# Optimization experiments

Hardware: AMD Instinct MI355X
Metric: run time of the kernel (lower is better)

Reference implementation:

```python
import jax, jax.numpy as jnp
import numpy as np

D = 128           # embed_dim
NUM_LAYERS = 2
N_CLASSES = 4
OUT_CELL = 64
SPEAKERS = 2
INPUT_DIMS = [768, 74, 35]
B, T = 32, 60


def setup_inputs() -> dict:
    key = jax.random.key(0)
    ks = jax.random.split(key, 24)
    inp = {}
    inp['x0'] = jax.random.normal(ks[0], (B, T, INPUT_DIMS[0]), jnp.float32)
    inp['x1'] = jax.random.normal(ks[1], (B, T, INPUT_DIMS[1]), jnp.float32)
    inp['x2'] = jax.random.normal(ks[2], (B, T, INPUT_DIMS[2]), jnp.float32)
    inp['smask'] = jax.random.normal(ks[3], (B, T, SPEAKERS), jnp.float32)  # argmax -> speaker ids
    # modality projections
    for i, d in enumerate(INPUT_DIMS):
        inp[f'Wp{i}'] = jax.random.normal(ks[4 + i], (d, D), jnp.float32) / np.float32(np.sqrt(d))
        inp[f'bp{i}'] = jnp.zeros((D,), jnp.float32)
    # shared PositionEmbedding (ModuleList([m]*3) shares params)
    inp['freq_emb'] = jax.random.normal(ks[7], (SPEAKERS, D), jnp.float32) * 0.1
    inp['phase_emb'] = jax.random.normal(ks[8], (SPEAKERS, D), jnp.float32)
    # shared QRNNCell (ModuleList([cell]*num_layers) shares params)
    inp['U_x'] = jnp.linalg.qr(jax.random.normal(ks[9], (D, D), jnp.float32))[0]
    inp['U_h'] = jnp.linalg.qr(jax.random.normal(ks[10], (D, D), jnp.float32))[0]
    inp['Lambda'] = jnp.float32(0.5)
    # QMeasurement kernel (real/imag parts of D measurement vectors)
    inp['kernel_r'] = jnp.eye(D, dtype=jnp.float32) + 0.05 * jax.random.normal(ks[11], (D, D), jnp.float32)
    inp['kernel_i'] = 0.05 * jax.random.normal(ks[12], (D, D), jnp.float32)
    # SimpleNet fc_out
    inp['W1'] = jax.random.normal(ks[13], (D, OUT_CELL), jnp.float32) / np.float32(np.sqrt(D))
    inp['b1'] = jnp.zeros((OUT_CELL,), jnp.float32)
    inp['W2'] = jax.random.normal(ks[14], (OUT_CELL, N_CLASSES), jnp.float32) / np.float32(np.sqrt(OUT_CELL))
    inp['b2'] = jnp.zeros((N_CLASSES,), jnp.float32)
    return inp


def _qmn_forward(x0, x1, x2, smask, Wp0, bp0, Wp1, bp1, Wp2, bp2,
                 freq_emb, phase_emb, U_x, U_h, Lambda,
                 kernel_r, kernel_i, W1, b1, W2, b2):
    xs = [x0, x1, x2]
    Ws = [(Wp0, bp0), (Wp1, bp1), (Wp2, bp2)]
    reps = [jax.nn.relu(x @ W + b) for x, (W, b) in zip(xs, Ws)]           # [B,T,D] each
    # mixture weights: softmax over per-modality L2 norms
    norms = jnp.concatenate([jnp.linalg.norm(r, axis=-1, keepdims=True) for r in reps], axis=-1)
    weights = jax.nn.softmax(norms, axis=-1)                               # [B,T,M]
    # shared phase embedding: phase = t * freq[speaker] + phase[speaker]
    ids = jnp.argmax(smask, axis=-1)                                       # [B,T] int
    pos = jnp.arange(T, dtype=jnp.float32)[None, :, None]                  # [1,T,1]
    phase = pos * freq_emb[ids] + phase_emb[ids]                           # [B,T,D]
    cosp, sinp = jnp.cos(phase), jnp.sin(phase)
    # mixed density matrices rho = sum_m w_m |v_m><v_m|
    rho_r = jnp.zeros((B, T, D, D), jnp.float32)
    rho_i = jnp.zeros((B, T, D, D), jnp.float32)
    for m, r in enumerate(reps):
        a = r / jnp.maximum(jnp.linalg.norm(r, axis=-1, keepdims=True), 1e-12)
        pr = a * cosp                                                       # real amplitude
        pi = a * sinp                                                       # imag amplitude
        w = weights[..., m][..., None, None]
        rho_r = rho_r + w * (jnp.einsum('btm,btn->btmn', pr, pr) + jnp.einsum('btm,btn->btmn', pi, pi))
        rho_i = rho_i + w * (jnp.einsum('btm,btn->btmn', pi, pr) - jnp.einsum('btm,btn->btmn', pr, pi))
    # time-major for scan
    sr = jnp.transpose(rho_r, (1, 0, 2, 3))                                # [T,B,D,D]
    si = jnp.transpose(rho_i, (1, 0, 2, 3))

    def cell(h, x):
        hr, hi = h
        xr, xi = x
        Xr = jnp.einsum('mp,bpq,nq->bmn', U_x, xr, U_x)
        Xi = jnp.einsum('mp,bpq,nq->bmn', U_x, xi, U_x)
        Hr = jnp.einsum('mp,bpq,nq->bmn', U_h, hr, U_h)
        Hi = jnp.einsum('mp,bpq,nq->bmn', U_h, hi, U_h)
        nr = Lambda * Hr + (1.0 - Lambda) * Xr
        ni = Lambda * Hi + (1.0 - Lambda) * Xi
        return (nr, ni), (nr, ni)

    h0 = (jnp.broadcast_to(jnp.eye(D, dtype=jnp.float32) / D, (B, D, D)),
          jnp.zeros((B, D, D), jnp.float32))
    for _ in range(NUM_LAYERS):  # same shared cell params each layer
        _, (sr, si) = jax.lax.scan(cell, h0, (sr, si))
    # QMeasurement: p_k = Re(v_k^dag rho v_k), unit-norm complex measurement vectors
    nrm = jnp.sqrt(jnp.sum(kernel_r**2 + kernel_i**2, axis=1, keepdims=True))
    vr = kernel_r / jnp.maximum(nrm, 1e-12)                                # [K,D], K=D
    vi = kernel_i / jnp.maximum(nrm, 1e-12)
    probs = (jnp.einsum('tbmn,km,kn->tbk', sr, vr, vr)
             + jnp.einsum('tbmn,km,kn->tbk', sr, vi, vi)
             - jnp.einsum('tbmn,km,kn->tbk', si, vr, vi)
             + jnp.einsum('tbmn,km,kn->tbk', si, vi, vr))                  # [T,B,D]
    # SimpleNet (dropout = identity at inference)
    hid = jax.nn.relu(probs @ W1 + b1)
    out = jnp.tanh(hid @ W2 + b2)                                          # [T,B,C]
    out = jnp.transpose(out, (1, 0, 2))                                    # [B,T,C]
    return jax.nn.log_softmax(out, axis=2)


def reference(x0, x1, x2, smask, Wp0, bp0, Wp1, bp1, Wp2, bp2,
              freq_emb, phase_emb, U_x, U_h, Lambda,
              kernel_r, kernel_i, W1, b1, W2, b2):
    return _qmn_forward(x0, x1, x2, smask, Wp0, bp0, Wp1, bp1, Wp2, bp2,
                        freq_emb, phase_emb, U_x, U_h, Lambda,
                        kernel_r, kernel_i, W1, b1, W2, b2)
```

## Files before the change

kernel.cpp:

```cpp
#include <hip/hip_runtime.h>


#define DB 32
#define DT 60
#define DD 128
#define BT (DB*DT)
#define SP 136

typedef unsigned short ushort_t;
typedef __attribute__((ext_vector_type(8))) __bf16 bf16x8;
typedef __attribute__((ext_vector_type(8))) unsigned short ushort8_t;
typedef __attribute__((ext_vector_type(4))) float  float4v;

__device__ __forceinline__ float bf2f(ushort_t u){
  union { unsigned int i; float f; } x; x.i = ((unsigned int)u) << 16; return x.f;
}
__device__ __forceinline__ ushort_t f2bf(float f){
  union { float f; unsigned int i; } x; x.f = f;
  unsigned int lsb = (x.i >> 16) & 1u;
  return (ushort_t)((x.i + 0x7FFFu + lsb) >> 16);
}
__device__ __forceinline__ unsigned int f2bfpk(float a, float b){
#if defined(__gfx950__) && __has_builtin(__builtin_amdgcn_cvt_pk_bf16_f32)
  auto v = __builtin_amdgcn_cvt_pk_bf16_f32(a, b);
  unsigned int r; __builtin_memcpy(&r, &v, 4); return r;
#else
  return (unsigned int)f2bf(a) | ((unsigned int)f2bf(b) << 16);
#endif
}
__device__ __forceinline__ void split2(float v, ushort_t& h, ushort_t& l){
  h = f2bf(v); l = f2bf(v - bf2f(h));
}

template<int RT, int CT, bool ALO, bool BLO>
__device__ __forceinline__ void gemm_t(const ushort_t* Ah, const ushort_t* Al,
                                       const ushort_t* Bh, const ushort_t* Bl,
                                       float4v* acc, int row0, int col0, int gma, int q)
{
  for (int ks = 0; ks < 4; ks++){
    int ko = ks*32 + q*8;
    bf16x8 aF[RT], aL[RT], bF[CT], bL[CT];
    #pragma unroll
    for (int R = 0; R < RT; R++){
      int row = row0 + 16*R + gma;
      aF[R] = *(const bf16x8*)&Ah[row*SP + ko];
      if (ALO) aL[R] = *(const bf16x8*)&Al[row*SP + ko];
    }
    #pragma unroll
    for (int C = 0; C < CT; C++){
      int row = col0 + 16*C + gma;
      bF[C] = *(const bf16x8*)&Bh[row*SP + ko];
      if (BLO) bL[C] = *(const bf16x8*)&Bl[row*SP + ko];
    }
    #pragma unroll
    for (int R = 0; R < RT; R++)
      #pragma unroll
      for (int C = 0; C < CT; C++){
        float4v c = acc[R*CT+C];
        c = __builtin_amdgcn_mfma_f32_16x16x32_bf16(aF[R], bF[C], c, 0, 0, 0);
        if (BLO) c = __builtin_amdgcn_mfma_f32_16x16x32_bf16(aF[R], bL[C], c, 0, 0, 0);
        if (ALO) c = __builtin_amdgcn_mfma_f32_16x16x32_bf16(aL[R], bF[C], c, 0, 0, 0);
        acc[R*CT+C] = c;
      }
  }
}

template<int RT, int CT>
__device__ __forceinline__ void emit_t(const float4v* acc, ushort_t* dst, int stride,
                                       int row0, int col0, int gma, int q){
  #pragma unroll
  for (int R = 0; R < RT; R++)
    #pragma unroll
    for (int C = 0; C < CT; C++){
      int c = col0 + 16*C + gma, r0 = row0 + 16*R + 4*q;
      uint2 o;
      o.x = f2bfpk(acc[R*CT+C][0], acc[R*CT+C][1]);
      o.y = f2bfpk(acc[R*CT+C][2], acc[R*CT+C][3]);
      *(uint2*)&dst[(size_t)c*stride + r0] = o;
    }
}
template<int RT, int CT>
__device__ __forceinline__ void emit_split_t(const float4v* acc, ushort_t* dh, ushort_t* dl, int stride,
                                             int row0, int col0, int gma, int q){
  #pragma unroll
  for (int R = 0; R < RT; R++)
    #pragma unroll
    for (int C = 0; C < CT; C++){
      int c = col0 + 16*C + gma, r0 = row0 + 16*R + 4*q;
      ushort4 hh, ll;
      split2(acc[R*CT+C][0], hh.x, ll.x); split2(acc[R*CT+C][1], hh.y, ll.y);
      split2(acc[R*CT+C][2], hh.z, ll.z); split2(acc[R*CT+C][3], hh.w, ll.w);
      *(ushort4*)&dh[(size_t)c*stride + r0] = hh;
      *(ushort4*)&dl[(size_t)c*stride + r0] = ll;
    }
}
template<int NT>
__device__ __forceinline__ void lds_load_mat(ushort_t* dst, const ushort_t* src, int tid){
  for (int i = tid*8; i < 16384; i += NT*8){
    int r = i >> 7, k = i & 127;
    *(ushort8_t*)&dst[r*SP + k] = *(const ushort8_t*)&src[i];
  }
}
template<int NT>
__device__ __forceinline__ void lds_load_rows16(ushort_t* dst, const ushort_t* src, int tid){
  for (int i = tid*8; i < 2048; i += NT*8){
    int r = i >> 7, k = i & 127;
    *(ushort8_t*)&dst[r*SP + k] = *(const ushort8_t*)&src[i];
  }
}
template<int NT>
__device__ __forceinline__ void lds_load_mat2(ushort_t* d0, const ushort_t* s0,
                                              ushort_t* d1, const ushort_t* s1, int tid){
  constexpr int CH = 16384/(NT*8);
  ushort8_t r0[CH], r1[CH];
  #pragma unroll
  for (int c = 0; c < CH; c++) r0[c] = *(const ushort8_t*)&s0[tid*8 + c*NT*8];
  #pragma unroll
  for (int c = 0; c < CH; c++) r1[c] = *(const ushort8_t*)&s1[tid*8 + c*NT*8];
  #pragma unroll
  for (int c = 0; c < CH; c++){
    int i = tid*8 + c*NT*8; int r = i >> 7, k = i & 127;
    *(ushort8_t*)&d0[r*SP + k] = r0[c];
  }
  #pragma unroll
  for (int c = 0; c < CH; c++){
    int i = tid*8 + c*NT*8; int r = i >> 7, k = i & 127;
    *(ushort8_t*)&d1[r*SP + k] = r1[c];
  }
}
template<int NT>
__device__ __forceinline__ void lds_store_mat(ushort_t* dst, const ushort_t* src, int tid){
  for (int i = tid*8; i < 16384; i += NT*8){
    int r = i >> 7, k = i & 127;
    *(ushort8_t*)&dst[i] = *(const ushort8_t*)&src[r*SP + k];
  }
}

__global__ void k_small(const float* Ux, const float* Uh, const float* kr, const float* ki,
                        const float* Wp0, const float* Wp1, const float* Wp2,
                        const float* x0, const float* x1, const float* x2,
                        ushort_t* UxTh, ushort_t* UxTl, ushort_t* UxH, ushort_t* UxL,
                        float* Vr, float* Vi,
                        ushort_t* PpH, ushort_t* PpL, ushort_t* PTh, ushort_t* PTl,
                        ushort_t* WT0h, ushort_t* WT0l, ushort_t* WT1h, ushort_t* WT1l,
                        ushort_t* WT2h, ushort_t* WT2l,
                        ushort_t* X0h, ushort_t* X0l, ushort_t* X1h, ushort_t* X1l,
                        ushort_t* X2h, ushort_t* X2l){
  int blk = blockIdx.x, d = threadIdx.x;
  if (blk < 128){
    int i = blk;
    float v = Ux[i*DD + d];
    ushort_t h, l; split2(v, h, l);
    UxTh[d*DD + i] = h; UxTl[d*DD + i] = l;
  } else if (blk < 256){
    __shared__ float red[DD];
    int k = blk - 128;
    float r = kr[k*DD+d], im = ki[k*DD+d];
    red[d] = r*r + im*im;
    __syncthreads();
    for (int s = 64; s > 0; s >>= 1){ if (d < s) red[d] += red[d+s]; __syncthreads(); }
    float nrm = fmaxf(sqrtf(red[0]), 1e-12f);
    Vr[k*DD+d] = r/nrm; Vi[k*DD+d] = im/nrm;
  } else if (blk < 384){
    int i = blk - 256;
    float v = Uh[i*DD + d];
    ushort_t h, l; split2(v, h, l);
    PpH[i*DD + d] = h;  PpL[i*DD + d] = l;
    PTh[d*DD + i] = h;  PTl[d*DD + i] = l;
  } else if (blk < 512){
    int dd2 = blk - 384;
    ushort_t h, l;
    for (int k = d; k < 768; k += 128){
      split2(Wp0[(size_t)k*DD + dd2], h, l);
      WT0h[(size_t)dd2*768 + k] = h; WT0l[(size_t)dd2*768 + k] = l;
    }
    { float v = (d < 74) ? Wp1[(size_t)d*DD + dd2] : 0.f;
      split2(v, h, l); WT1h[dd2*128 + d] = h; WT1l[dd2*128 + d] = l; }
    { float v = (d < 35) ? Wp2[(size_t)d*DD + dd2] : 0.f;
      split2(v, h, l); WT2h[dd2*128 + d] = h; WT2l[dd2*128 + d] = l; }
    { split2(Ux[(size_t)dd2*DD + d], h, l);
      UxH[dd2*DD + d] = h; UxL[dd2*DD + d] = l; }
  } else {
    int bt = blk - 512;
    ushort_t h, l;
    const float* r0 = x0 + (size_t)bt*768;
    #pragma unroll
    for (int j = 0; j < 6; j++){
      split2(r0[j*128 + d], h, l);
      X0h[(size_t)bt*768 + j*128 + d] = h;
      X0l[(size_t)bt*768 + j*128 + d] = l;
    }
    float v1 = (d < 74) ? x1[(size_t)bt*74 + d] : 0.f;
    split2(v1, h, l);
    X1h[(size_t)bt*128 + d] = h; X1l[(size_t)bt*128 + d] = l;
    float v2 = (d < 35) ? x2[(size_t)bt*35 + d] : 0.f;
    split2(v2, h, l);
    X2h[(size_t)bt*128 + d] = h; X2l[(size_t)bt*128 + d] = l;
  }
}

__global__ __launch_bounds__(512,1) void k_proj(
    const ushort_t* X0h, const ushort_t* X0l, const ushort_t* X1h, const ushort_t* X1l,
    const ushort_t* X2h, const ushort_t* X2l,
    const ushort_t* WT0h, const ushort_t* WT0l, const ushort_t* WT1h, const ushort_t* WT1l,
    const ushort_t* WT2h, const ushort_t* WT2l,
    const float* bp1, const float* bp2,
    float* Rpart, float* Reps)
{
  __shared__ ushort_t Ah[128*SP], Al[128*SP], Bh[128*SP], Bl[128*SP];
  int blk = blockIdx.x;
  int m, tile, ch;
  if (blk < 90){ m = 0; tile = blk/6; ch = blk%6; }
  else if (blk < 105){ m = 1; tile = blk-90; ch = 0; }
  else { m = 2; tile = blk-105; ch = 0; }
  int bt0 = tile*128;
  int tid = threadIdx.x;
  int w = tid >> 6, lane = tid & 63, gma = lane & 15, q = lane >> 4;
  int row0 = 32*(w >> 1), col0 = 64*(w & 1);
  const ushort_t* Wh_ = (m==0)? WT0h : (m==1)? WT1h : WT2h;
  const ushort_t* Wl_ = (m==0)? WT0l : (m==1)? WT1l : WT2l;
  const ushort_t* Xh_ = (m==0)? X0h : (m==1)? X1h : X2h;
  const ushort_t* Xl_ = (m==0)? X0l : (m==1)? X1l : X2l;
  int KX = (m==0)? 768 : 128;
  for (int i = tid*8; i < 16384; i += 4096){
    int r = i >> 7, k = i & 127;
    *(ushort8_t*)&Ah[r*SP + k] = *(const ushort8_t*)&Wh_[(size_t)r*KX + ch*128 + k];
    *(ushort8_t*)&Al[r*SP + k] = *(const ushort8_t*)&Wl_[(size_t)r*KX + ch*128 + k];
    *(ushort8_t*)&Bh[r*SP + k] = *(const ushort8_t*)&Xh_[(size_t)(bt0+r)*KX + ch*128 + k];
    *(ushort8_t*)&Bl[r*SP + k] = *(const ushort8_t*)&Xl_[(size_t)(bt0+r)*KX + ch*128 + k];
  }
  __syncthreads();
  float4v acc[8];
  #pragma unroll
  for (int i = 0; i < 8; i++) acc[i] = (float4v){0.f,0.f,0.f,0.f};
  gemm_t<2,4,true,true>(Ah, Al, Bh, Bl, acc, row0, col0, gma, q);
  if (m == 0){
    #pragma unroll
    for (int R = 0; R < 2; R++)
      #pragma unroll
      for (int C = 0; C < 4; C++){
        int c = col0 + 16*C + gma, r0 = row0 + 16*R + 4*q;
        float4 o;
        o.x = acc[R*4+C][0]; o.y = acc[R*4+C][1];
        o.z = acc[R*4+C][2]; o.w = acc[R*4+C][3];
        *(float4*)&Rpart[((size_t)ch*BT + bt0 + c)*128 + r0] = o;
      }
  } else {
    const float* bp = (m==1)? bp1 : bp2;
    #pragma unroll
    for (int R = 0; R < 2; R++){
      int r0 = row0 + 16*R + 4*q;
      float4 bv = *(const float4*)&bp[r0];
      #pragma unroll
      for (int C = 0; C < 4; C++){
        int c = col0 + 16*C + gma;
        float4v a = acc[R*4+C];
        float4 o;
        o.x = fmaxf(a[0]+bv.x, 0.f); o.y = fmaxf(a[1]+bv.y, 0.f);
        o.z = fmaxf(a[2]+bv.z, 0.f); o.w = fmaxf(a[3]+bv.w, 0.f);
        *(float4*)&Reps[(size_t)(bt0 + c)*384 + m*128 + r0] = o;
      }
    }
  }
}

__global__ __launch_bounds__(128) void k_mix(const float* Rpart, const float* Reps,
    const float* bp0, const float* smask,
    const float* freq, const float* phem, ushort_t* PsH, ushort_t* PsL, float* Wgt)
{
  __shared__ float part[2][3];
  int bt = blockIdx.x; int t = bt % DT;
  int d = threadIdx.x;
  float r0v = bp0[d];
  #pragma unroll
  for (int ch = 0; ch < 6; ch++)
    r0v += Rpart[((size_t)ch*BT + bt)*128 + d];
  r0v = fmaxf(r0v, 0.f);
  float r1v = Reps[(size_t)bt*384 + 128 + d];
  float r2v = Reps[(size_t)bt*384 + 256 + d];
  float s0 = r0v*r0v, s1 = r1v*r1v, s2 = r2v*r2v;
  #pragma unroll
  for (int off = 1; off < 64; off <<= 1){
    s0 += __shfl_xor(s0, off, 64);
    s1 += __shfl_xor(s1, off, 64);
    s2 += __shfl_xor(s2, off, 64);
  }
  int wv = d >> 6;
  if ((d & 63) == 0){ part[wv][0] = s0; part[wv][1] = s1; part[wv][2] = s2; }
  __syncthreads();
  float n0 = sqrtf(part[0][0] + part[1][0]);
  float n1 = sqrtf(part[0][1] + part[1][1]);
  float n2 = sqrtf(part[0][2] + part[1][2]);
  float mx = fmaxf(n0, fmaxf(n1, n2));
  float e0 = expf(n0-mx), e1 = expf(n1-mx), e2 = expf(n2-mx);
  float einv = 1.f/(e0+e1+e2);
  if (d < 3) Wgt[bt*3+d] = (d==0?e0:(d==1?e1:e2))*einv;
  float sm0 = smask[bt*2], sm1 = smask[bt*2+1];
  int id = (sm1 > sm0) ? 1 : 0;
  float ph = (float)t * freq[id*DD+d] + phem[id*DD+d];
  float cp = cosf(ph), sp = sinf(ph);
  float a0 = r0v / fmaxf(n0, 1e-12f);
  float a1 = r1v / fmaxf(n1, 1e-12f);
  float a2 = r2v / fmaxf(n2, 1e-12f);
  ushort_t h, l;
  split2(a0*cp, h, l); PsH[((size_t)0*BT + bt)*DD + d] = h; PsL[((size_t)0*BT + bt)*DD + d] = l;
  split2(a1*cp, h, l); PsH[((size_t)1*BT + bt)*DD + d] = h; PsL[((size_t)1*BT + bt)*DD + d] = l;
  split2(a2*cp, h, l); PsH[((size_t)2*BT + bt)*DD + d] = h; PsL[((size_t)2*BT + bt)*DD + d] = l;
  split2(a0*sp, h, l); PsH[((size_t)3*BT + bt)*DD + d] = h; PsL[((size_t)3*BT + bt)*DD + d] = l;
  split2(a1*sp, h, l); PsH[((size_t)4*BT + bt)*DD + d] = h; PsL[((size_t)4*BT + bt)*DD + d] = l;
  split2(a2*sp, h, l); PsH[((size_t)5*BT + bt)*DD + d] = h; PsL[((size_t)5*BT + bt)*DD + d] = l;
}

__global__ __launch_bounds__(512,1) void k_qtrans(const ushort_t* UxH, const ushort_t* UxL,
                                                  const ushort_t* PsH, const ushort_t* PsL,
                                                  ushort_t* Qb){
  __shared__ ushort_t Ah[128*SP], Al[128*SP], Bh[128*SP], Bl[128*SP];
  int blk = blockIdx.x;
  int tid = threadIdx.x;
  int w = tid >> 6, lane = tid & 63, gma = lane & 15, q = lane >> 4;
  int row0 = 32*(w >> 1), col0 = 64*(w & 1);
  size_t rbase = (size_t)blk*128*128;
  lds_load_mat<512>(Ah, UxH, tid);
  lds_load_mat<512>(Al, UxL, tid);
  lds_load_mat<512>(Bh, PsH + rbase, tid);
  lds_load_mat<512>(Bl, PsL + rbase, tid);
  __syncthreads();
  float4v acc[8];
  #pragma unroll
  for (int i = 0; i < 8; i++) acc[i] = (float4v){0.f,0.f,0.f,0.f};
  gemm_t<2,4,true,true>(Ah, Al, Bh, Bl, acc, row0, col0, gma, q);
  emit_t<2,4>(acc, Qb + rbase, 128, row0, col0, gma, q);
}

__global__ __launch_bounds__(256,2) void k_pow2v2(ushort_t* PpH, ushort_t* PpL,
                                                  ushort_t* PTh, ushort_t* PTl, int s){
  __shared__ ushort_t Ah[128*SP], Al[128*SP], Bh[16*SP], Bl[16*SP];
  int blk = blockIdx.x;
  int which = blk >> 3, sl = blk & 7;
  size_t src = (size_t)(s-1)*16384, dst = (size_t)s*16384;
  int tid = threadIdx.x;
  int w = tid >> 6, lane = tid & 63, gma = lane & 15, q = lane >> 4;
  int row0 = 32*w;
  int gcol0 = sl*16;
  const ushort_t *A_h, *A_l, *B_h, *B_l; ushort_t *D_h, *D_l;
  if (which == 0){ A_h = PTh+src; A_l = PTl+src; B_h = PpH+src; B_l = PpL+src;
                   D_h = PpH+dst; D_l = PpL+dst; }
  else           { A_h = PpH+src; A_l = PpL+src; B_h = PTh+src; B_l = PTl+src;
                   D_h = PTh+dst; D_l = PTl+dst; }
  lds_load_mat<256>(Ah, A_h, tid);
  lds_load_mat<256>(Al, A_l, tid);
  lds_load_rows16<256>(Bh, B_h + (size_t)gcol0*128, tid);
  lds_load_rows16<256>(Bl, B_l + (size_t)gcol0*128, tid);
  __syncthreads();
  float4v acc[2];
  acc[0] = (float4v){0.f,0.f,0.f,0.f};
  acc[1] = (float4v){0.f,0.f,0.f,0.f};
  gemm_t<2,1,true,true>(Ah, Al, Bh, Bl, acc, row0, 0, gma, q);
  emit_split_t<2,1>(acc, D_h, D_l, 128, row0, gcol0, gma, q);
}

__global__ __launch_bounds__(512,1) void k_gchain(const ushort_t* PpH, const ushort_t* PpL,
                                                  const ushort_t* PTh, const ushort_t* PTl,
                                                  ushort_t* GTh, ushort_t* GTl){
  __shared__ ushort_t Ah[128*SP], Al[128*SP], Bh[128*SP], Bl[128*SP];
  int t = blockIdx.x;
  int tid = threadIdx.x;
  int w = tid >> 6, lane = tid & 63, gma = lane & 15, q = lane >> 4;
  int row0 = 32*(w >> 1), col0 = 64*(w & 1);
  size_t gslot = (size_t)t * 16384;
  if (t == 0){
    for (int i = tid*4; i < 16384; i += 2048){
      int r = i >> 7, k = i & 127;
      ushort4 zz; zz.x = zz.y = zz.z = zz.w = 0;
      *(ushort4*)&GTl[gslot + i] = zz;
      ushort4 oh;
      oh.x = (r == (k+0)) ? (ushort_t)0x3F80 : (ushort_t)0;
      oh.y = (r == (k+1)) ? (ushort_t)0x3F80 : (ushort_t)0;
      oh.z = (r == (k+2)) ? (ushort_t)0x3F80 : (ushort_t)0;
      oh.w = (r == (k+3)) ? (ushort_t)0x3F80 : (ushort_t)0;
      *(ushort4*)&GTh[gslot + i] = oh;
    }
    return;
  }
  int b0 = __ffs(t) - 1;
  int rem = t & ~(1 << b0);
  if (rem == 0){
    size_t ps = (size_t)b0 * 16384;
    for (int i = tid*4; i < 16384; i += 2048){
      *(ushort4*)&GTh[gslot + i] = *(const ushort4*)&PTh[ps + i];
      *(ushort4*)&GTl[gslot + i] = *(const ushort4*)&PTl[ps + i];
    }
    return;
  }
  lds_load_mat<512>(Ah, PpH + (size_t)b0*16384, tid);
  lds_load_mat<512>(Al, PpL + (size_t)b0*16384, tid);
  while (rem){
    int k = __ffs(rem) - 1;
    rem &= ~(1 << k);
    lds_load_mat<512>(Bh, PTh + (size_t)k*16384, tid);
    lds_load_mat<512>(Bl, PTl + (size_t)k*16384, tid);
    __syncthreads();
    float4v acc[8];
    #pragma unroll
    for (int i = 0; i < 8; i++) acc[i] = (float4v){0.f,0.f,0.f,0.f};
    if (rem){
      gemm_t<2,4,true,true>(Bh, Bl, Ah, Al, acc, row0, col0, gma, q);
      __syncthreads();
      emit_split_t<2,4>(acc, Ah, Al, SP, row0, col0, gma, q);
      __syncthreads();
    } else {
      gemm_t<2,4,true,true>(Ah, Al, Bh, Bl, acc, row0, col0, gma, q);
      emit_split_t<2,4>(acc, GTh + gslot, GTl + gslot, 128, row0, col0, gma, q);
    }
  }
}

__global__ __launch_bounds__(256,1) void k_precompMW(const ushort_t* GTh, const ushort_t* GTl,
                                                     const ushort_t* UxTh, const ushort_t* UxTl,
                                                     const float* Vr, const float* Vi,
                                                     ushort_t* Mh, ushort_t* Wh){
  __shared__ ushort_t Bh[128*SP], Bl[128*SP], Ah[128*SP], Al[128*SP];
  int blk = blockIdx.x;
  int tid = threadIdx.x;
  int w = tid >> 6, lane = tid & 63, gma = lane & 15, q = lane >> 4;
  int row0 = 64*(w >> 1), col0 = 64*(w & 1);
  if (blk < 60){
    int t = blk;
    lds_load_mat<256>(Bh, GTh + (size_t)t*16384, tid);
    lds_load_mat<256>(Bl, GTl + (size_t)t*16384, tid);
    lds_load_mat<256>(Ah, UxTh, tid);
    lds_load_mat<256>(Al, UxTl, tid);
    __syncthreads();
    float4v acc[16];
    #pragma unroll
    for (int i = 0; i < 16; i++) acc[i] = (float4v){0.f,0.f,0.f,0.f};
    gemm_t<4,4,true,true>(Ah, Al, Bh, Bl, acc, row0, col0, gma, q);
    __syncthreads();
    emit_split_t<4,4>(acc, Ah, Al, SP, row0, col0, gma, q);
    __syncthreads();
    #pragma unroll
    for (int i = 0; i < 16; i++) acc[i] = (float4v){0.f,0.f,0.f,0.f};
    gemm_t<4,4,true,true>(Bh, Bl, Ah, Al, acc, row0, col0, gma, q);
    #pragma unroll
    for (int R = 0; R < 4; R++)
      #pragma unroll
      for (int C = 0; C < 4; C++){
        int c = col0 + 16*C + gma, r0 = row0 + 16*R + 4*q;
        uint2 o;
        o.x = f2bfpk(acc[R*4+C][0], acc[R*4+C][1]);
        o.y = f2bfpk(acc[R*4+C][2], acc[R*4+C][3]);
        *(uint2*)&Mh[(size_t)t*16384 + c*128 + r0] = o;
      }
  } else {
    int bx = blk - 60;
    int t = bx >> 1, which = bx & 1;
    lds_load_mat<256>(Ah, GTh + (size_t)t*16384, tid);
    lds_load_mat<256>(Al, GTl + (size_t)t*16384, tid);
    const float* V = which ? Vi : Vr;
    for (int i = tid; i < 16384; i += 256){
      int r = i >> 7, k = i & 127;
      ushort_t h, l; split2(V[i], h, l);
      Bh[r*SP + k] = h; Bl[r*SP + k] = l;
    }
    __syncthreads();
    float4v acc[16];
    #pragma unroll
    for (int i = 0; i < 16; i++) acc[i] = (float4v){0.f,0.f,0.f,0.f};
    gemm_t<4,4,true,true>(Ah, Al, Bh, Bl, acc, row0, col0, gma, q);
    #pragma unroll
    for (int R = 0; R < 4; R++)
      #pragma unroll
      for (int C = 0; C < 4; C++){
        int c = col0 + 16*C + gma, r0 = row0 + 16*R + 4*q;
        uint2 o;
        o.x = f2bfpk(acc[R*4+C][0], acc[R*4+C][1]);
        o.y = f2bfpk(acc[R*4+C][2], acc[R*4+C][3]);
        *(uint2*)&Wh[(size_t)bx*16384 + c*128 + r0] = o;
      }
  }
}

__global__ __launch_bounds__(512,1) void k_vtrans(const ushort_t* GTh, const ushort_t* Qb, ushort_t* At){
  __shared__ ushort_t Ah[128*SP];
  __shared__ ushort_t Bs[192*SP];
  int t = blockIdx.x;
  int tid = threadIdx.x;
  int w = tid >> 6, lane = tid & 63, gma = lane & 15, q = lane >> 4;
  int row0 = (w & 3)*32, col0 = (w >> 2)*96;
  lds_load_mat<512>(Ah, GTh + (size_t)t*16384, tid);
  for (int i = tid*8; i < 192*128; i += 4096){
    int m = i >> 7, k = i & 127;
    int j = m >> 5, b = m & 31;
    *(ushort8_t*)&Bs[m*SP + k] =
      *(const ushort8_t*)&Qb[((size_t)(j*BT) + b*DT + t)*DD + k];
  }
  __syncthreads();
  float4v acc[12];
  #pragma unroll
  for (int i = 0; i < 12; i++) acc[i] = (float4v){0.f,0.f,0.f,0.f};
  gemm_t<2,6,false,false>(Ah, Ah, Bs, Bs, acc, row0, col0, gma, q);
  emit_t<2,6>(acc, At + (size_t)t*24576, 128, row0, col0, gma, q);
}

__global__ __launch_bounds__(256) void k_zbuild(ushort_t* S, const ushort_t* At,
                                                const float* Wgt, const float* lamp){
  __shared__ ushort_t As[2][6*DD];
  __shared__ float wl[2][3];
  int blk = blockIdx.x;
  int b = blk >> 5, sl2 = blk & 31;
  int tid = threadIdx.x;
  int r = sl2*4 + (tid >> 6);
  int c = (tid*2) & 127;
  float lam = lamp[0];
  float z0 = 0.f, z1 = 0.f;
  size_t off = (size_t)sl2*512 + tid*2;
  ushort4 pre;
  float wpre = 0.f;
  int jj0 = 0, n0 = 0;
  if (tid < 192){
    int i = tid*4;
    jj0 = i >> 7; n0 = i & 127;
    pre = *(const ushort4*)&At[(size_t)(jj0*32 + b)*128 + n0];
  }
  if (tid < 3) wpre = Wgt[(b*DT)*3 + tid];
  for (int t = 0; t < DT; t++){
    int cur = t & 1;
    if (tid < 192) *(ushort4*)&As[cur][tid*4] = pre;
    if (tid < 3) wl[cur][tid] = wpre;
    __syncthreads();
    if (t+1 < DT){
      if (tid < 192)
        pre = *(const ushort4*)&At[(size_t)(t+1)*24576 + (size_t)(jj0*32 + b)*128 + n0];
      if (tid < 3) wpre = Wgt[(b*DT + t+1)*3 + tid];
    }
    float ar[6];
    #pragma unroll
    for (int jj = 0; jj < 6; jj++) ar[jj] = bf2f(As[cur][jj*128 + r]);
    float w0 = wl[cur][0], w1 = wl[cur][1], w2 = wl[cur][2];
    float cb[6];
    cb[0] = w0*(ar[0]+ar[3]); cb[1] = w1*(ar[1]+ar[4]); cb[2] = w2*(ar[2]+ar[5]);
    cb[3] = w0*(ar[3]-ar[0]); cb[4] = w1*(ar[4]-ar[1]); cb[5] = w2*(ar[5]-ar[2]);
    float y0 = 0.f, y1 = 0.f;
    #pragma unroll
    for (int jj = 0; jj < 6; jj++){
      unsigned int a2 = *(const unsigned int*)&As[cur][jj*128 + c];
      float w_ = cb[jj];
      y0 += w_*bf2f((ushort_t)(a2 & 0xFFFF));
      y1 += w_*bf2f((ushort_t)(a2 >> 16));
    }
    z0 = lam*z0 + y0; z1 = lam*z1 + y1;
    *(unsigned int*)&S[((size_t)(t*32 + b))*16384 + off] = f2bfpk(z0, z1);
  }
}

__global__ __launch_bounds__(512,4) void k_conjmid(ushort_t* S, const ushort_t* Mh,
                                                   const float* lamp){
  __shared__ ushort_t Bh[128*SP], Zs[128*SP];
  int blk = blockIdx.x;
  int t = blk >> 5;
  size_t slot = (size_t)blk * 16384;
  int tid = threadIdx.x;
  int w = tid >> 6, lane = tid & 63, gma = lane & 15, q = lane >> 4;
  int row0 = 32*(w >> 1), col0 = 64*(w & 1);
  lds_load_mat2<512>(Zs, S + slot, Bh, Mh + (size_t)t*16384, tid);
  __syncthreads();
  float lam = lamp[0];
  float oml = 1.f - lam;
  float ct = powf(lam, (float)(t+1)) / 128.f;
  float4v acc[8];
  #pragma unroll
  for (int i = 0; i < 8; i++) acc[i] = (float4v){0.f,0.f,0.f,0.f};
  gemm_t<2,4,false,false>(Zs, Zs, Bh, Bh, acc, row0, col0, gma, q);
  __syncthreads();
  emit_t<2,4>(acc, Zs, SP, row0, col0, gma, q);
  __syncthreads();
  #pragma unroll
  for (int i = 0; i < 8; i++) acc[i] = (float4v){0.f,0.f,0.f,0.f};
  gemm_t<2,4,false,false>(Zs, Zs, Bh, Bh, acc, row0, col0, gma, q);
  __syncthreads();
  #pragma unroll
  for (int R = 0; R < 2; R++)
    #pragma unroll
    for (int C = 0; C < 4; C++){
      int c = col0 + 16*C + gma, r0 = row0 + 16*R + 4*q;
      float v0 = oml*acc[R*4+C][0] + ((c == r0+0) ? ct : 0.f);
      float v1 = oml*acc[R*4+C][1] + ((c == r0+1) ? ct : 0.f);
      float v2 = oml*acc[R*4+C][2] + ((c == r0+2) ? ct : 0.f);
      float v3 = oml*acc[R*4+C][3] + ((c == r0+3) ? ct : 0.f);
      uint2 o; o.x = f2bfpk(v0, v1); o.y = f2bfpk(v2, v3);
      *(uint2*)&Zs[(size_t)c*SP + r0] = o;
    }
  __syncthreads();
  lds_store_mat<512>(S + slot, Zs, tid);
}

__device__ __forceinline__ void prefix_ph2(uint2& buf, bool doload,
                                           const ushort_t* Snext, ushort_t* Scur,
                                           float* a, float lam){
  uint2 u = buf;
  if (doload) buf = *(const uint2*)Snext;
  a[0] = lam*a[0] + bf2f((ushort_t)(u.x & 0xFFFF));
  a[1] = lam*a[1] + bf2f((ushort_t)(u.x >> 16));
  a[2] = lam*a[2] + bf2f((ushort_t)(u.y & 0xFFFF));
  a[3] = lam*a[3] + bf2f((ushort_t)(u.y >> 16));
  uint2 o;
  o.x = f2bfpk(a[0], a[1]); o.y = f2bfpk(a[2], a[3]);
  *(uint2*)Scur = o;
}
__global__ __launch_bounds__(128) void k_prefix(ushort_t* S, const float* lamp){
  int blk = blockIdx.x;
  int chain = blk >> 5, slab = blk & 31;
  int tid = threadIdx.x;
  size_t off = (size_t)slab*512 + tid*4;
  float lam = lamp[0];
  float a[4];
  #pragma unroll
  for (int i = 0; i < 4; i++) a[i] = 0.f;
  size_t addr = (size_t)chain*16384 + off;
  const size_t step = (size_t)32*16384;
  uint2 b0 = *(const uint2*)&S[addr];
  uint2 b1 = *(const uint2*)&S[addr + step];
  uint2 b2 = *(const uint2*)&S[addr + 2*step];
  uint2 b3 = *(const uint2*)&S[addr + 3*step];
  uint2 b4 = *(const uint2*)&S[addr + 4*step];
  uint2 b5 = *(const uint2*)&S[addr + 5*step];
  for (int t = 0; t < DT; t += 6){
    prefix_ph2(b0, t+6  < DT, &S[addr + 6*step], &S[addr], a, lam); addr += step;
    prefix_ph2(b1, t+7  < DT, &S[addr + 6*step], &S[addr], a, lam); addr += step;
    prefix_ph2(b2, t+8  < DT, &S[addr + 6*step], &S[addr], a, lam); addr += step;
    prefix_ph2(b3, t+9  < DT, &S[addr + 6*step], &S[addr], a, lam); addr += step;
    prefix_ph2(b4, t+10 < DT, &S[addr + 6*step], &S[addr], a, lam); addr += step;
    prefix_ph2(b5, t+11 < DT, &S[addr + 6*step], &S[addr], a, lam); addr += step;
  }
}

__global__ __launch_bounds__(512,2) void k_meas(const ushort_t* S, const ushort_t* Wh,
                                                const float* lamp, float* Probs){
  __shared__ ushort_t Vs[128*SP], Cs[128*SP];
  __shared__ float Pd[64];
  int raw = blockIdx.x;
  int tb = (raw & 7) | ((raw >> 4) << 3);
  int h  = (raw >> 3) & 1;
  int t = tb >> 5;
  int tid = threadIdx.x;
  int w = tid >> 6, lane = tid & 63, gma = lane & 15, q = lane >> 4;
  int row0 = 16*(w >> 1);
  int col0 = 64*(w & 1);
  size_t slot = (size_t)tb * 16384;
  size_t wbase = (size_t)(t*2) * 16384;
  ushort8_t creg[4], vreg[4];
  #pragma unroll
  for (int c = 0; c < 4; c++)
    creg[c] = *(const ushort8_t*)&S[slot + tid*8 + c*4096];
  #pragma unroll
  for (int c = 0; c < 4; c++){
    int i = tid*8 + c*4096;
    int r = i >> 7, k = i & 127;
    size_t gsrc = wbase + ((r < 64) ? 0 : 16384) + (size_t)(64*h + (r & 63))*128 + k;
    vreg[c] = *(const ushort8_t*)&Wh[gsrc];
  }
  if (tid < 64) Pd[tid] = 0.f;
  #pragma unroll
  for (int c = 0; c < 4; c++){
    int i = tid*8 + c*4096;
    int r = i >> 7, k = i & 127;
    *(ushort8_t*)&Cs[r*SP + k] = creg[c];
  }
  #pragma unroll
  for (int c = 0; c < 4; c++){
    int i = tid*8 + c*4096;
    int r = i >> 7, k = i & 127;
    *(ushort8_t*)&Vs[r*SP + k] = vreg[c];
  }
  __syncthreads();
  float4v acc[8];
  #pragma unroll
  for (int i = 0; i < 8; i++) acc[i] = (float4v){0.f,0.f,0.f,0.f};
  #pragma unroll
  for (int ks = 0; ks < 4; ks++){
    int ko = ks*32 + q*8;
    bf16x8 aF0 = *(const bf16x8*)&Vs[(row0 + gma)*SP + ko];
    bf16x8 aF1 = *(const bf16x8*)&Vs[(row0 + 64 + gma)*SP + ko];
    bf16x8 bF[4];
    #pragma unroll
    for (int C = 0; C < 4; C++)
      bF[C] = *(const bf16x8*)&Cs[(col0 + 16*C + gma)*SP + ko];
    #pragma unroll
    for (int C = 0; C < 4; C++){
      acc[C]   = __builtin_amdgcn_mfma_f32_16x16x32_bf16(aF0, bF[C], acc[C],   0, 0, 0);
      acc[4+C] = __builtin_amdgcn_mfma_f32_16x16x32_bf16(aF1, bF[C], acc[4+C], 0, 0, 0);
    }
  }
  #pragma unroll
  for (int j = 0; j < 4; j++){
    int kr = row0 + 4*q + j;
    float s = 0.f;
    #pragma unroll
    for (int C = 0; C < 4; C++){
      int m = col0 + 16*C + gma;
      float w0 = bf2f(Vs[kr*SP + m]);
      float w1 = bf2f(Vs[(kr + 64)*SP + m]);
      s += acc[C][j]*(w0 + w1) + acc[4+C][j]*(w1 - w0);
    }
    #pragma unroll
    for (int off = 1; off < 16; off <<= 1)
      s += __shfl_xor(s, off, 64);
    if (gma == 0) atomicAdd(&Pd[kr], s);
  }
  __syncthreads();
  if (tid < 64){
    float lam = lamp[0];
    float ct = powf(lam, (float)(t+1)) / 128.f;
    Probs[(size_t)tb*DD + 64*h + tid] = (1.f - lam)*Pd[tid] + ct;
  }
}

__global__ __launch_bounds__(64) void k_head(const float* Probs, const float* W1, const float* b1,
                        const float* W2, const float* b2, float* out)
{
  __shared__ float ps[DD];
  __shared__ float hid[64];
  __shared__ float ov[4];
  int tb = blockIdx.x;
  int tid = threadIdx.x;
  ps[tid] = Probs[(size_t)tb*DD + tid];
  ps[tid+64] = Probs[(size_t)tb*DD + 64 + tid];
  __syncthreads();
  float acc = b1[tid];
  for (int dd = 0; dd < DD; dd++) acc += ps[dd]*W1[dd*64 + tid];
  hid[tid] = fmaxf(acc, 0.f);
  __syncthreads();
  if (tid < 4){
    float o = b2[tid];
    for (int j = 0; j < 64; j++) o += hid[j]*W2[j*4 + tid];
    ov[tid] = tanhf(o);
  }
  __syncthreads();
  if (tid == 0){
    float m = fmaxf(fmaxf(ov[0],ov[1]), fmaxf(ov[2],ov[3]));
    float lse = logf(expf(ov[0]-m)+expf(ov[1]-m)+expf(ov[2]-m)+expf(ov[3]-m));
    int t = tb >> 5, b = tb & 31;
    float* o = out + ((size_t)(b*DT + t))*4;
    o[0] = ov[0]-m-lse; o[1] = ov[1]-m-lse;
    o[2] = ov[2]-m-lse; o[3] = ov[3]-m-lse;
  }
}

extern "C" void kernel_launch(void* const* d_in, const int* in_sizes, int n_in,
                              void* d_out, int out_size, void* d_ws, size_t ws_size,
                              hipStream_t stream)
{
  const float* x0    = (const float*)d_in[0];
  const float* x1    = (const float*)d_in[1];
  const float* x2    = (const float*)d_in[2];
  const float* smask = (const float*)d_in[3];
  const float* Wp0   = (const float*)d_in[4];
  const float* bp0   = (const float*)d_in[5];
  const float* Wp1   = (const float*)d_in[6];
  const float* bp1   = (const float*)d_in[7];
  const float* Wp2   = (const float*)d_in[8];
  const float* bp2   = (const float*)d_in[9];
  const float* freq  = (const float*)d_in[10];
  const float* phem  = (const float*)d_in[11];
  const float* Ux    = (const float*)d_in[12];
  const float* Uh    = (const float*)d_in[13];
  const float* lamp  = (const float*)d_in[14];
  const float* kr    = (const float*)d_in[15];
  const float* ki    = (const float*)d_in[16];
  const float* W1    = (const float*)d_in[17];
  const float* b1    = (const float*)d_in[18];
  const float* W2    = (const float*)d_in[19];
  const float* b2    = (const float*)d_in[20];

  char* ws = (char*)d_ws;
  auto alignup = [](size_t x){ return (x + 255) & ~(size_t)255; };
  size_t off = 0;
  ushort_t* S   = (ushort_t*)(ws + off); off = alignup(off + (size_t)1920*16384*sizeof(ushort_t));
  ushort_t* Qb  = (ushort_t*)(ws + off); off = alignup(off + (size_t)6*BT*DD*sizeof(ushort_t));
  float* Rpart  = (float*)(ws + off);    off = alignup(off + (size_t)6*BT*DD*sizeof(float));
  float* Reps   = (float*)(ws + off);    off = alignup(off + (size_t)BT*384*sizeof(float));
  ushort_t* PsH = (ushort_t*)(ws + off); off = alignup(off + (size_t)6*BT*DD*sizeof(ushort_t));
  ushort_t* PsL = (ushort_t*)(ws + off); off = alignup(off + (size_t)6*BT*DD*sizeof(ushort_t));
  ushort_t* X0h = (ushort_t*)(ws + off); off = alignup(off + (size_t)BT*768*sizeof(ushort_t));
  ushort_t* X0l = (ushort_t*)(ws + off); off = alignup(off + (size_t)BT*768*sizeof(ushort_t));
  ushort_t* X1h = (ushort_t*)(ws + off); off = alignup(off + (size_t)BT*128*sizeof(ushort_t));
  ushort_t* X1l = (ushort_t*)(ws + off); off = alignup(off + (size_t)BT*128*sizeof(ushort_t));
  ushort_t* X2h = (ushort_t*)(ws + off); off = alignup(off + (size_t)BT*128*sizeof(ushort_t));
  ushort_t* X2l = (ushort_t*)(ws + off); off = alignup(off + (size_t)BT*128*sizeof(ushort_t));
  float* Wgt    = (float*)(ws + off);    off = alignup(off + (size_t)BT*3*sizeof(float));
  float* Vr     = (float*)(ws + off);    off = alignup(off + (size_t)DD*DD*sizeof(float));
  float* Vi     = (float*)(ws + off);    off = alignup(off + (size_t)DD*DD*sizeof(float));
  ushort_t* UxTh = (ushort_t*)(ws + off); off = alignup(off + (size_t)DD*DD*sizeof(ushort_t));
  ushort_t* UxTl = (ushort_t*)(ws + off); off = alignup(off + (size_t)DD*DD*sizeof(ushort_t));
  ushort_t* UxH = (ushort_t*)(ws + off); off = alignup(off + (size_t)DD*DD*sizeof(ushort_t));
  ushort_t* UxL = (ushort_t*)(ws + off); off = alignup(off + (size_t)DD*DD*sizeof(ushort_t));
  float* Probs  = (float*)(ws + off);    off = alignup(off + (size_t)BT*DD*sizeof(float));
  ushort_t* PpH = (ushort_t*)(ws + off); off = alignup(off + (size_t)6*16384*sizeof(ushort_t));
  ushort_t* PpL = (ushort_t*)(ws + off); off = alignup(off + (size_t)6*16384*sizeof(ushort_t));
  ushort_t* PTh = (ushort_t*)(ws + off); off = alignup(off + (size_t)6*16384*sizeof(ushort_t));
  ushort_t* PTl = (ushort_t*)(ws + off); off = alignup(off + (size_t)6*16384*sizeof(ushort_t));
  ushort_t* Mh  = (ushort_t*)(ws + off); off = alignup(off + (size_t)60*16384*sizeof(ushort_t));
  ushort_t* Wmh = (ushort_t*)(ws + off); off = alignup(off + (size_t)120*16384*sizeof(ushort_t));
  ushort_t* GTh = (ushort_t*)(ws + off); off = alignup(off + (size_t)60*16384*sizeof(ushort_t));
  ushort_t* GTl = (ushort_t*)(ws + off); off = alignup(off + (size_t)60*16384*sizeof(ushort_t));
  ushort_t* At  = (ushort_t*)(ws + off); off = alignup(off + (size_t)60*24576*sizeof(ushort_t));
  ushort_t* WT0h = (ushort_t*)(ws + off); off = alignup(off + (size_t)128*768*sizeof(ushort_t));
  ushort_t* WT0l = (ushort_t*)(ws + off); off = alignup(off + (size_t)128*768*sizeof(ushort_t));
  ushort_t* WT1h = (ushort_t*)(ws + off); off = alignup(off + (size_t)128*128*sizeof(ushort_t));
  ushort_t* WT1l = (ushort_t*)(ws + off); off = alignup(off + (size_t)128*128*sizeof(ushort_t));
  ushort_t* WT2h = (ushort_t*)(ws + off); off = alignup(off + (size_t)128*128*sizeof(ushort_t));
  ushort_t* WT2l = (ushort_t*)(ws + off); off = alignup(off + (size_t)128*128*sizeof(ushort_t));
  (void)ws_size; (void)in_sizes; (void)n_in; (void)out_size;

  k_small<<<512 + BT, 128, 0, stream>>>(Ux, Uh, kr, ki, Wp0, Wp1, Wp2, x0, x1, x2,
                                        UxTh, UxTl, UxH, UxL, Vr, Vi,
                                        PpH, PpL, PTh, PTl,
                                        WT0h, WT0l, WT1h, WT1l, WT2h, WT2l,
                                        X0h, X0l, X1h, X1l, X2h, X2l);
  k_proj<<<120, 512, 0, stream>>>(X0h, X0l, X1h, X1l, X2h, X2l,
                                  WT0h, WT0l, WT1h, WT1l, WT2h, WT2l,
                                  bp1, bp2, Rpart, Reps);
  k_mix<<<BT, 128, 0, stream>>>(Rpart, Reps, bp0, smask, freq, phem, PsH, PsL, Wgt);
  k_qtrans<<<90, 512, 0, stream>>>(UxH, UxL, PsH, PsL, Qb);
  for (int s = 1; s <= 5; s++)
    k_pow2v2<<<16, 256, 0, stream>>>(PpH, PpL, PTh, PTl, s);
  k_gchain<<<60, 512, 0, stream>>>(PpH, PpL, PTh, PTl, GTh, GTl);
  k_precompMW<<<180, 256, 0, stream>>>(GTh, GTl, UxTh, UxTl, Vr, Vi, Mh, Wmh);
  k_vtrans<<<60, 512, 0, stream>>>(GTh, Qb, At);
  k_zbuild<<<1024, 256, 0, stream>>>(S, At, Wgt, lamp);
  k_conjmid<<<1920, 512, 0, stream>>>(S, Mh, lamp);
  k_prefix<<<1024, 128, 0, stream>>>(S, lamp);
  k_meas<<<3840, 512, 0, stream>>>(S, Wmh, lamp, Probs);
  k_head<<<BT, 64, 0, stream>>>(Probs, W1, b1, W2, b2, (float*)d_out);
}
```

Measured before the change: 314.5 us.

## Process four batch slots per block in conjmid and meas to reuse weights

k_conjmid and k_meas now each handle four consecutive (t,b) slots per block instead of one, so the per-t Mh / Wmh matrices are loaded into LDS once and reused across the four slots. The next slot's state is prefetched into registers while the current one is computed. Grid sizes shrink by four, from 1920 to 480 and from 3840 to 960 blocks. In exchange there is less parallelism, conjmid's occupancy hint drops from 4 to 2 blocks per CU, and extra barriers are added per iteration.

New measurement: 310.8 us. About the same (-1.2%).

```diff
diff --git a/kernel.cpp b/kernel.cpp
--- a/kernel.cpp
+++ b/kernel.cpp
@@ -553,45 +553,64 @@
   }
 }
 
-__global__ __launch_bounds__(512,4) void k_conjmid(ushort_t* S, const ushort_t* Mh,
+__global__ __launch_bounds__(512,2) void k_conjmid(ushort_t* S, const ushort_t* Mh,
                                                    const float* lamp){
   __shared__ ushort_t Bh[128*SP], Zs[128*SP];
-  int blk = blockIdx.x;
-  int t = blk >> 5;
-  size_t slot = (size_t)blk * 16384;
+  int raw = blockIdx.x;
+  int g = raw & 7, t = raw >> 3;
   int tid = threadIdx.x;
   int w = tid >> 6, lane = tid & 63, gma = lane & 15, q = lane >> 4;
   int row0 = 32*(w >> 1), col0 = 64*(w & 1);
-  lds_load_mat2<512>(Zs, S + slot, Bh, Mh + (size_t)t*16384, tid);
+  size_t slot0 = (size_t)(t*32 + g*4) * 16384;
+  lds_load_mat2<512>(Zs, S + slot0, Bh, Mh + (size_t)t*16384, tid);
   __syncthreads();
   float lam = lamp[0];
   float oml = 1.f - lam;
   float ct = powf(lam, (float)(t+1)) / 128.f;
-  float4v acc[8];
-  #pragma unroll
-  for (int i = 0; i < 8; i++) acc[i] = (float4v){0.f,0.f,0.f,0.f};
-  gemm_t<2,4,false,false>(Zs, Zs, Bh, Bh, acc, row0, col0, gma, q);
-  __syncthreads();
-  emit_t<2,4>(acc, Zs, SP, row0, col0, gma, q);
-  __syncthreads();
-  #pragma unroll
-  for (int i = 0; i < 8; i++) acc[i] = (float4v){0.f,0.f,0.f,0.f};
-  gemm_t<2,4,false,false>(Zs, Zs, Bh, Bh, acc, row0, col0, gma, q);
-  __syncthreads();
-  #pragma unroll
-  for (int R = 0; R < 2; R++)
-    #pragma unroll
-    for (int C = 0; C < 4; C++){
-      int c = col0 + 16*C + gma, r0 = row0 + 16*R + 4*q;
-      float v0 = oml*acc[R*4+C][0] + ((c == r0+0) ? ct : 0.f);
-      float v1 = oml*acc[R*4+C][1] + ((c == r0+1) ? ct : 0.f);
-      float v2 = oml*acc[R*4+C][2] + ((c == r0+2) ? ct : 0.f);
-      float v3 = oml*acc[R*4+C][3] + ((c == r0+3) ? ct : 0.f);
-      uint2 o; o.x = f2bfpk(v0, v1); o.y = f2bfpk(v2, v3);
-      *(uint2*)&Zs[(size_t)c*SP + r0] = o;
-    }
-  __syncthreads();
-  lds_store_mat<512>(S + slot, Zs, tid);
+  for (int ib = 0; ib < 4; ib++){
+    size_t slot = slot0 + (size_t)ib*16384;
+    ushort8_t znext[4];
+    if (ib < 3){
+      #pragma unroll
+      for (int c = 0; c < 4; c++)
+        znext[c] = *(const ushort8_t*)&S[slot + 16384 + tid*8 + c*4096];
+    }
+    float4v acc[8];
+    #pragma unroll
+    for (int i = 0; i < 8; i++) acc[i] = (float4v){0.f,0.f,0.f,0.f};
+    gemm_t<2,4,false,false>(Zs, Zs, Bh, Bh, acc, row0, col0, gma, q);
+    __syncthreads();
+    emit_t<2,4>(acc, Zs, SP, row0, col0, gma, q);
+    __syncthreads();
+    #pragma unroll
+    for (int i = 0; i < 8; i++) acc[i] = (float4v){0.f,0.f,0.f,0.f};
+    gemm_t<2,4,false,false>(Zs, Zs, Bh, Bh, acc, row0, col0, gma, q);
+    __syncthreads();
+    #pragma unroll
+    for (int R = 0; R < 2; R++)
+      #pragma unroll
+      for (int C = 0; C < 4; C++){
+        int c = col0 + 16*C + gma, r0 = row0 + 16*R + 4*q;
+        float v0 = oml*acc[R*4+C][0] + ((c == r0+0) ? ct : 0.f);
+        float v1 = oml*acc[R*4+C][1] + ((c == r0+1) ? ct : 0.f);
+        float v2 = oml*acc[R*4+C][2] + ((c == r0+2) ? ct : 0.f);
+        float v3 = oml*acc[R*4+C][3] + ((c == r0+3) ? ct : 0.f);
+        uint2 o; o.x = f2bfpk(v0, v1); o.y = f2bfpk(v2, v3);
+        *(uint2*)&Zs[(size_t)c*SP + r0] = o;
+      }
+    __syncthreads();
+    lds_store_mat<512>(S + slot, Zs, tid);
+    if (ib < 3){
+      __syncthreads();
+      #pragma unroll
+      for (int c = 0; c < 4; c++){
+        int i = tid*8 + c*4096;
+        int r = i >> 7, k = i & 127;
+        *(ushort8_t*)&Zs[r*SP + k] = znext[c];
+      }
+      __syncthreads();
+    }
+  }
 }
 
 __device__ __forceinline__ void prefix_ph2(uint2& buf, bool doload,
@@ -639,19 +658,19 @@
   __shared__ ushort_t Vs[128*SP], Cs[128*SP];
   __shared__ float Pd[64];
   int raw = blockIdx.x;
-  int tb = (raw & 7) | ((raw >> 4) << 3);
-  int h  = (raw >> 3) & 1;
-  int t = tb >> 5;
+  int g = raw & 7;
+  int h = (raw >> 3) & 1;
+  int t = raw >> 4;
   int tid = threadIdx.x;
   int w = tid >> 6, lane = tid & 63, gma = lane & 15, q = lane >> 4;
   int row0 = 16*(w >> 1);
   int col0 = 64*(w & 1);
-  size_t slot = (size_t)tb * 16384;
   size_t wbase = (size_t)(t*2) * 16384;
+  size_t slot0 = (size_t)(t*32 + g*4) * 16384;
   ushort8_t creg[4], vreg[4];
   #pragma unroll
   for (int c = 0; c < 4; c++)
-    creg[c] = *(const ushort8_t*)&S[slot + tid*8 + c*4096];
+    creg[c] = *(const ushort8_t*)&S[slot0 + tid*8 + c*4096];
   #pragma unroll
   for (int c = 0; c < 4; c++){
     int i = tid*8 + c*4096;
@@ -665,53 +684,66 @@
     int i = tid*8 + c*4096;
     int r = i >> 7, k = i & 127;
     *(ushort8_t*)&Cs[r*SP + k] = creg[c];
-  }
-  #pragma unroll
-  for (int c = 0; c < 4; c++){
-    int i = tid*8 + c*4096;
-    int r = i >> 7, k = i & 127;
     *(ushort8_t*)&Vs[r*SP + k] = vreg[c];
   }
   __syncthreads();
-  float4v acc[8];
-  #pragma unroll
-  for (int i = 0; i < 8; i++) acc[i] = (float4v){0.f,0.f,0.f,0.f};
-  #pragma unroll
-  for (int ks = 0; ks < 4; ks++){
-    int ko = ks*32 + q*8;
-    bf16x8 aF0 = *(const bf16x8*)&Vs[(row0 + gma)*SP + ko];
-    bf16x8 aF1 = *(const bf16x8*)&Vs[(row0 + 64 + gma)*SP + ko];
-    bf16x8 bF[4];
-    #pragma unroll
-    for (int C = 0; C < 4; C++)
-      bF[C] = *(const bf16x8*)&Cs[(col0 + 16*C + gma)*SP + ko];
-    #pragma unroll
-    for (int C = 0; C < 4; C++){
-      acc[C]   = __builtin_amdgcn_mfma_f32_16x16x32_bf16(aF0, bF[C], acc[C],   0, 0, 0);
-      acc[4+C] = __builtin_amdgcn_mfma_f32_16x16x32_bf16(aF1, bF[C], acc[4+C], 0, 0, 0);
-    }
-  }
-  #pragma unroll
-  for (int j = 0; j < 4; j++){
-    int kr = row0 + 4*q + j;
-    float s = 0.f;
-    #pragma unroll
-    for (int C = 0; C < 4; C++){
-      int m = col0 + 16*C + gma;
-      float w0 = bf2f(Vs[kr*SP + m]);
-      float w1 = bf2f(Vs[(kr + 64)*SP + m]);
-      s += acc[C][j]*(w0 + w1) + acc[4+C][j]*(w1 - w0);
-    }
-    #pragma unroll
-    for (int off = 1; off < 16; off <<= 1)
-      s += __shfl_xor(s, off, 64);
-    if (gma == 0) atomicAdd(&Pd[kr], s);
-  }
-  __syncthreads();
-  if (tid < 64){
-    float lam = lamp[0];
-    float ct = powf(lam, (float)(t+1)) / 128.f;
-    Probs[(size_t)tb*DD + 64*h + tid] = (1.f - lam)*Pd[tid] + ct;
+  float lam = lamp[0];
+  float ct = powf(lam, (float)(t+1)) / 128.f;
+  for (int ib = 0; ib < 4; ib++){
+    if (ib < 3){
+      size_t snx = slot0 + (size_t)(ib+1)*16384;
+      #pragma unroll
+      for (int c = 0; c < 4; c++)
+        creg[c] = *(const ushort8_t*)&S[snx + tid*8 + c*4096];
+    }
+    float4v acc[8];
+    #pragma unroll
+    for (int i = 0; i < 8; i++) acc[i] = (float4v){0.f,0.f,0.f,0.f};
+    #pragma unroll
+    for (int ks = 0; ks < 4; ks++){
+      int ko = ks*32 + q*8;
+      bf16x8 aF0 = *(const bf16x8*)&Vs[(row0 + gma)*SP + ko];
+      bf16x8 aF1 = *(const bf16x8*)&Vs[(row0 + 64 + gma)*SP + ko];
+      bf16x8 bF[4];
+      #pragma unroll
+      for (int C = 0; C < 4; C++)
+        bF[C] = *(const bf16x8*)&Cs[(col0 + 16*C + gma)*SP + ko];
+      #pragma unroll
+      for (int C = 0; C < 4; C++){
+        acc[C]   = __builtin_amdgcn_mfma_f32_16x16x32_bf16(aF0, bF[C], acc[C],   0, 0, 0);
+        acc[4+C] = __builtin_amdgcn_mfma_f32_16x16x32_bf16(aF1, bF[C], acc[4+C], 0, 0, 0);
+      }
+    }
+    #pragma unroll
+    for (int j = 0; j < 4; j++){
+      int kr = row0 + 4*q + j;
+      float s = 0.f;
+      #pragma unroll
+      for (int C = 0; C < 4; C++){
+        int m = col0 + 16*C + gma;
+        float w0 = bf2f(Vs[kr*SP + m]);
+        float w1 = bf2f(Vs[(kr + 64)*SP + m]);
+        s += acc[C][j]*(w0 + w1) + acc[4+C][j]*(w1 - w0);
+      }
+      #pragma unroll
+      for (int off = 1; off < 16; off <<= 1)
+        s += __shfl_xor(s, off, 64);
+      if (gma == 0) atomicAdd(&Pd[kr], s);
+    }
+    __syncthreads();
+    if (tid < 64){
+      Probs[(size_t)(t*32 + g*4 + ib)*DD + 64*h + tid] = (1.f - lam)*Pd[tid] + ct;
+      Pd[tid] = 0.f;
+    }
+    if (ib < 3){
+      #pragma unroll
+      for (int c = 0; c < 4; c++){
+        int i = tid*8 + c*4096;
+        int r = i >> 7, k = i & 127;
+        *(ushort8_t*)&Cs[r*SP + k] = creg[c];
+      }
+    }
+    __syncthreads();
   }
 }
 
@@ -828,8 +860,8 @@
   k_precompMW<<<180, 256, 0, stream>>>(GTh, GTl, UxTh, UxTl, Vr, Vi, Mh, Wmh);
   k_vtrans<<<60, 512, 0, stream>>>(GTh, Qb, At);
   k_zbuild<<<1024, 256, 0, stream>>>(S, At, Wgt, lamp);
-  k_conjmid<<<1920, 512, 0, stream>>>(S, Mh, lamp);
+  k_conjmid<<<480, 512, 0, stream>>>(S, Mh, lamp);
   k_prefix<<<1024, 128, 0, stream>>>(S, lamp);
-  k_meas<<<3840, 512, 0, stream>>>(S, Wmh, lamp, Probs);
+  k_meas<<<960, 512, 0, stream>>>(S, Wmh, lamp, Probs);
   k_head<<<BT, 64, 0, stream>>>(Probs, W1, b1, W2, b2, (float*)d_out);
 }
```
